# Kernel optimization log

Measured on AMD Instinct MI355X. Metric: run time of the kernel, lower is better.

## Reference

```python
import jax, jax.numpy as jnp
from jax import lax
import numpy as np

B, H, W = 8, 160, 256
C, K = 700, 250
N_BINS = 750
N_HIST, N_JIT = 30, 60
N_FRAMES = N_HIST + N_JIT
MAGIC = 400.0 / (750.0 - 500.0 + 500.0)


def setup_inputs() -> dict:
    key = jax.random.key(0)
    ks = jax.random.split(key, 10)
    n_pix = H * W
    return {
        "batched_image": jax.random.normal(ks[0], (B, H, W), jnp.float32),
        "batched_spikes": jax.random.uniform(ks[1], (B, C, N_BINS), jnp.float32),
        "eye_movements": jax.random.randint(ks[2], (B, N_JIT, 2), 0, 15),
        "time_mask": jax.random.uniform(ks[3], (B, N_BINS - K), jnp.float32),
        "forward_sel": jax.random.randint(ks[4], (B, N_BINS, 2), 0, N_FRAMES),
        "forward_weights": jax.random.uniform(ks[5], (B, N_BINS, 2), jnp.float32),
        # scale filters so the generator signal stays O(1) under exp() nonlinearity
        "stacked_flat_spat_filters": jax.random.normal(ks[6], (C, n_pix), jnp.float32) / np.sqrt(n_pix).astype(np.float32),
        "stacked_timecourse_filters": jax.random.normal(ks[7], (C, K), jnp.float32) / np.sqrt(K).astype(np.float32),
        "precomputed_feedback_gensig": 0.1 * jax.random.normal(ks[8], (B, C, N_BINS - K + 1), jnp.float32),
        "precomputed_history_frames": jax.random.normal(ks[9], (B, N_HIST, C), jnp.float32),
    }


def _jitter(image, eye_movements):
    # image: (B,H,W); eye_movements: (B,F,2) int shifts. Gather with zero fill.
    dy, dx = eye_movements[..., 0], eye_movements[..., 1]
    rows = jnp.arange(H)[None, None, :] + dy[:, :, None]      # (B,F,H)
    cols = jnp.arange(W)[None, None, :] + dx[:, :, None]      # (B,F,W)
    vr = (rows >= 0) & (rows < H)
    vc = (cols >= 0) & (cols < W)
    rc = jnp.clip(rows, 0, H - 1)
    cc = jnp.clip(cols, 0, W - 1)
    bidx = jnp.arange(image.shape[0])[:, None, None, None]
    jit = image[bidx, rc[:, :, :, None], cc[:, :, None, :]]   # (B,F,H,W)
    mask = (vr[:, :, :, None] & vc[:, :, None, :]).astype(image.dtype)
    return jit * mask


def reference(batched_image, batched_spikes, eye_movements, time_mask,
              forward_sel, forward_weights, stacked_flat_spat_filters,
              stacked_timecourse_filters, precomputed_feedback_gensig,
              precomputed_history_frames):
    b = batched_image.shape[0]
    # eye-movement jitter (gather)
    jit = _jitter(batched_image, eye_movements)                       # (B,Fj,H,W)
    jit_flat = jit.reshape(b, -1, H * W)                              # (B,Fj,P)
    spat_j = jnp.einsum('cp,bfp->bfc', stacked_flat_spat_filters, jit_flat)
    spat = jnp.concatenate([precomputed_history_frames, spat_j], axis=1)  # (B,Ftot,C)
    # interval-overlap time upsample: each bin mixes <=2 frames
    t = forward_sel.shape[1]
    gath = jnp.take_along_axis(spat, forward_sel.reshape(b, t * 2, 1), axis=1)
    gath = gath.reshape(b, t, 2, -1)                                  # (B,T,2,C)
    upsampled = jnp.einsum('btjc,btj->bct', gath, forward_weights)    # (B,C,T)
    # grouped (depthwise) conv1d, valid, no flip (cross-correlation like torch)
    time_filt = lax.conv_general_dilated(
        upsampled, stacked_timecourse_filters[:, None, :],
        window_strides=(1,), padding='VALID',
        dimension_numbers=('NCH', 'OIH', 'NCH'), feature_group_count=C)  # (B,C,T-K+1)
    gen_sig = time_filt + precomputed_feedback_gensig
    g = gen_sig[:, :, :-1]
    s = batched_spikes[:, :, K:]
    loss = jnp.exp(g) - s * g                                          # Poisson NLL (unnormed)
    loss = loss * time_mask[:, None, :] * MAGIC
    return jnp.sum(loss, axis=(1, 2))
```

## Files before the change

### kernel.cpp

```cpp
#include <hip/hip_runtime.h>
#include <hip/hip_bf16.h>
#include <math.h>

#define BB    8
#define HH    160
#define WW    256
#define CC    700
#define KK    250
#define NBINS 750
#define NHIST 30
#define NJIT  60
#define NFRM  90
#define PP    (HH*WW)
#define TOUT  500
#define MAGIC (400.0f/750.0f)

#define MPAD   512
#define NPAD   768
#define KPTOT  640
#define KSPLIT 32
#define KPZ    20
#define BSCALE     64.0f
#define INV_BSCALE (1.0f/64.0f)
#define PA_BLKS (32*20)
#define PB_BLKS (48*20)

typedef __attribute__((ext_vector_type(8))) short short8;
typedef __attribute__((ext_vector_type(4))) float f32x4;

__device__ __forceinline__ unsigned char f2fp8(float x) {
    x = fminf(fmaxf(x, -440.f), 440.f);
    unsigned u = __builtin_bit_cast(unsigned, x);
    unsigned s = (u >> 24) & 0x80u;
    int e = (u >> 23) & 0xFF;
    if (e < 121) return (unsigned char)s;
    unsigned u2 = u + 0x7FFFFu + ((u >> 20) & 1u);
    int e2 = (u2 >> 23) & 0xFF;
    unsigned m = (u2 >> 20) & 7u;
    if (e2 > 135 || (e2 == 135 && m == 7u)) return (unsigned char)(s | 0x7E);
    return (unsigned char)(s | ((unsigned)(e2 - 120) << 3) | m);
}

__device__ __forceinline__ unsigned pk4_fp8(float a, float b, float c, float d) {
#if __has_builtin(__builtin_amdgcn_cvt_pk_fp8_f32)
    int v = __builtin_amdgcn_cvt_pk_fp8_f32(a, b, 0, false);
    v = __builtin_amdgcn_cvt_pk_fp8_f32(c, d, v, true);
    return (unsigned)v;
#else
    return (unsigned)f2fp8(a) | ((unsigned)f2fp8(b) << 8)
         | ((unsigned)f2fp8(c) << 16) | ((unsigned)f2fp8(d) << 24);
#endif
}

__device__ __forceinline__ void gload16(const void* g, void* l) {
    __builtin_amdgcn_global_load_lds(
        (const __attribute__((address_space(1))) unsigned int*)g,
        (__attribute__((address_space(3))) unsigned int*)l, 16, 0, 0);
}

__device__ __forceinline__ int SWZ(int X) { return X ^ (((X >> 8) & 7) << 4); }

__device__ __forceinline__ int FRX(int r, int pl) {
    return ((pl >> 6) << 10) | ((((pl >> 3) & 3) * 16 + r) << 4)
         | (((pl >> 5) & 1) << 3) | (pl & 7);
}

__global__ __launch_bounds__(256) void pack_ab(
    const float* __restrict__ img, const int* __restrict__ eye,
    const float* __restrict__ filt,
    unsigned char* __restrict__ Ap, unsigned char* __restrict__ Bp)
{
    __shared__ unsigned char lds[8192];
    const int t = threadIdx.x, w = t >> 6, l = t & 63;
    const int bid = blockIdx.x;

    if (bid < PA_BLKS) {
        const int mt = bid / 20, ch4 = bid % 20;
        int rbv[4], rdy[4], rdx[4]; bool rok[4];
        #pragma unroll
        for (int sub = 0; sub < 4; ++sub) {
            int r = sub*4 + w, m = mt*16 + r;
            rok[sub] = (m < 480);
            int b = 0, dy = 0, dx = 0;
            if (rok[sub]) {
                b = m / 60; int f = m % 60;
                dy = eye[(b*NJIT + f)*2 + 0];
                dx = eye[(b*NJIT + f)*2 + 1];
            }
            rbv[sub] = b; rdy[sub] = dy; rdx[sub] = dx;
        }
        for (int q = 0; q < 4; ++q) {
            const int ch = ch4*4 + q;
            const int kbase = ch * 512;
            #pragma unroll
            for (int sub = 0; sub < 4; ++sub) {
                const int r = sub*4 + w;
                const float* imgb = img + (size_t)rbv[sub]*PP;
                const int dx = rdx[sub];
                #pragma unroll
                for (int h = 0; h < 2; ++h) {
                    const int ir = (kbase >> 8) + h + rdy[sub];
                    const bool ok = rok[sub] && (ir < HH);
                    float4 v = make_float4(0.f,0.f,0.f,0.f);
                    if (ok) v = *(const float4*)(imgb + ir*WW + 4*l);
                    unsigned pk = pk4_fp8(v.x, v.y, v.z, v.w);
                    const int plb = h*256;
                    if (!ok || l >= 60)
                        *(unsigned*)(lds + SWZ(FRX(r, plb + 4*l))) = 0u;
                    if (ok) {
                        #pragma unroll
                        for (int j = 0; j < 4; ++j) {
                            int pc = 4*l + j - dx;
                            if (pc >= 0)
                                lds[SWZ(FRX(r, plb + pc))] =
                                    (unsigned char)(pk >> (8*j));
                        }
                    }
                }
            }
            __syncthreads();
            unsigned char* outp = Ap + ((size_t)mt*KPTOT + ch*8)*1024;
            #pragma unroll
            for (int i = 0; i < 2; ++i) {
                int X = i*4096 + t*16;
                short8 v = *(const short8*)(lds + SWZ(X));
                *(short8*)(outp + X) = v;
            }
            __syncthreads();
        }
    } else {
        const int bb = bid - PA_BLKS;
        const int nt = bb / 20, ch4 = bb % 20;
        for (int q = 0; q < 4; ++q) {
            const int ch = ch4*4 + q;
            const int kbase = ch * 512;
            #pragma unroll
            for (int sub = 0; sub < 4; ++sub) {
                int r = sub*4 + w, n = nt*16 + r;
                float4 va = make_float4(0.f,0.f,0.f,0.f), vb = va;
                if (n < CC) {
                    const float* rowp = filt + (size_t)n*PP + kbase;
                    va = *(const float4*)(rowp + l*4);
                    vb = *(const float4*)(rowp + l*4 + 256);
                }
                unsigned da = pk4_fp8(va.x*BSCALE, va.y*BSCALE, va.z*BSCALE, va.w*BSCALE);
                unsigned db = pk4_fp8(vb.x*BSCALE, vb.y*BSCALE, vb.z*BSCALE, vb.w*BSCALE);
                int Xa = FRX(r, 4*l);
                *(unsigned*)(lds + SWZ(Xa)) = da;
                *(unsigned*)(lds + SWZ(Xa + (4 << 10))) = db;
            }
            __syncthreads();
            unsigned char* outp = Bp + ((size_t)nt*KPTOT + ch*8)*1024;
            #pragma unroll
            for (int i = 0; i < 2; ++i) {
                int X = i*4096 + t*16;
                short8 v = *(const short8*)(lds + SWZ(X));
                *(short8*)(outp + X) = v;
            }
            __syncthreads();
        }
    }
}

__global__ __launch_bounds__(256) void gemm_f8(
    const unsigned char* __restrict__ Ap, const unsigned char* __restrict__ Bp,
    __hip_bfloat16* __restrict__ part)
{
    __shared__ unsigned char As[8192];
    __shared__ unsigned char Bs[8192];

    const int t = threadIdx.x, l = t & 63, w = t >> 6;
    const int bid = blockIdx.x;
    const int g   = bid >> 3;
    const int z   = (bid & 7) + 8*(g / 24);
    const int tt  = g % 24;
    const int mtile = tt / 6, ntile = tt % 6;
    const int wr = w >> 1, wc = w & 1;

    f32x4 acc[4][4] = {};

    for (int step = 0; step < KPZ; ++step) {
        const size_t kp = (size_t)z*KPZ + step;
        const int tb0 = w*2, tb1 = w*2 + 1;
        gload16(Ap + ((size_t)(mtile*8 + tb0)*KPTOT + kp)*1024 + l*16, As + tb0*1024);
        gload16(Ap + ((size_t)(mtile*8 + tb1)*KPTOT + kp)*1024 + l*16, As + tb1*1024);
        gload16(Bp + ((size_t)(ntile*8 + tb0)*KPTOT + kp)*1024 + l*16, Bs + tb0*1024);
        gload16(Bp + ((size_t)(ntile*8 + tb1)*KPTOT + kp)*1024 + l*16, Bs + tb1*1024);
        __syncthreads();

        ulonglong2 a[4], b[4];
        #pragma unroll
        for (int i = 0; i < 4; ++i)
            a[i] = *(const ulonglong2*)(As + (wr*4 + i)*1024 + l*16);
        #pragma unroll
        for (int j = 0; j < 4; ++j)
            b[j] = *(const ulonglong2*)(Bs + (wc*4 + j)*1024 + l*16);
        #pragma unroll
        for (int i = 0; i < 4; ++i)
            #pragma unroll
            for (int j = 0; j < 4; ++j) {
                acc[i][j] = __builtin_amdgcn_mfma_f32_16x16x32_fp8_fp8(
                    (long long)a[i].x, (long long)b[j].x, acc[i][j], 0, 0, 0);
                acc[i][j] = __builtin_amdgcn_mfma_f32_16x16x32_fp8_fp8(
                    (long long)a[i].y, (long long)b[j].y, acc[i][j], 0, 0, 0);
            }
        __syncthreads();
    }

    const int rbase = (l >> 4)*4, cl = l & 15;
    #pragma unroll
    for (int i = 0; i < 4; ++i)
        #pragma unroll
        for (int j = 0; j < 4; ++j) {
            int m = mtile*128 + wr*64 + i*16 + rbase;
            int n = ntile*128 + wc*64 + j*16 + cl;
            __hip_bfloat16* p = part + ((size_t)z*MPAD + m)*NPAD + n;
            #pragma unroll
            for (int r = 0; r < 4; ++r)
                p[(size_t)r*NPAD] = __float2bfloat16(acc[i][j][r]);
        }
}

__global__ __launch_bounds__(256) void build_spat(
    const float* __restrict__ hist, const __hip_bfloat16* __restrict__ part,
    float* __restrict__ spatT)
{
    int idx = blockIdx.x*256 + threadIdx.x;
    if (idx >= BB*NFRM*CC) return;
    int c   = idx % CC;
    int rem = idx / CC;
    int fr  = rem % NFRM;
    int b   = rem / NFRM;
    float v;
    if (fr < NHIST) {
        v = hist[(b*NHIST + fr)*CC + c];
    } else {
        int m = b*NJIT + (fr - NHIST);
        v = 0.f;
        #pragma unroll
        for (int kp = 0; kp < KSPLIT; ++kp)
            v += __bfloat162float(part[((size_t)kp*MPAD + m)*NPAD + c]);
        v *= INV_BSCALE;
    }
    spatT[((size_t)b*CC + c)*NFRM + fr] = v;
}

__global__ __launch_bounds__(64) void conv_loss(
    const float* __restrict__ spatT, const int* __restrict__ sel,
    const float* __restrict__ wts,  const float* __restrict__ tc,
    const float* __restrict__ fb,   const float* __restrict__ spk,
    const float* __restrict__ tmask, float* __restrict__ lpart)
{
    __shared__ float tcs[256];
    __shared__ float spc[96];
    __shared__ float ups[864];

    const int lane = threadIdx.x;
    const int c = blockIdx.x;
    const int b = blockIdx.y;

    for (int k = lane; k < 256; k += 64)
        tcs[k] = (k < KK) ? tc[c*KK + k] : 0.f;
    {
        const float* spT = spatT + (size_t)(b*CC + c)*NFRM;
        for (int i = lane; i < NFRM; i += 64) spc[i] = spT[i];
    }
    __syncthreads();

    for (int tt = lane; tt < 768; tt += 64) {
        float v = 0.f;
        if (tt < NBINS) {
            int base = (b*NBINS + tt);
            int2   s2 = *(const int2*)  (sel + base*2);
            float2 w2 = *(const float2*)(wts + base*2);
            v = w2.x * spc[s2.x] + w2.y * spc[s2.y];
        }
        ups[tt + (tt >> 3)] = v;
    }
    __syncthreads();

    const int t0 = lane * 8;
    float u[16];
    #pragma unroll
    for (int j = 0; j < 16; ++j) { int q = t0 + j; u[j] = ups[q + (q >> 3)]; }

    float acc[8] = {};
    #pragma unroll 4
    for (int kc = 0; kc < 248; kc += 8) {
        #pragma unroll
        for (int kk = 0; kk < 8; ++kk) {
            float w2 = tcs[kc + kk];
            #pragma unroll
            for (int j = 0; j < 8; ++j) acc[j] += w2 * u[kk + j];
        }
        #pragma unroll
        for (int j = 0; j < 8; ++j) u[j] = u[j + 8];
        #pragma unroll
        for (int j = 0; j < 8; ++j) {
            int q = t0 + kc + 16 + j;
            u[j + 8] = ups[q + (q >> 3)];
        }
    }
    #pragma unroll
    for (int kk = 0; kk < 8; ++kk) {
        float w2 = tcs[248 + kk];
        #pragma unroll
        for (int j = 0; j < 8; ++j) acc[j] += w2 * u[kk + j];
    }

    const size_t bc = (size_t)b*CC + c;
    const float* fbp = fb  + bc*(TOUT+1);
    const float* sp  = spk + bc*NBINS + KK;
    const float* tm  = tmask + (size_t)b*TOUT;
    float lsum = 0.f;
    #pragma unroll
    for (int j = 0; j < 8; ++j) {
        int tt = t0 + j;
        if (tt < TOUT) {
            float g  = acc[j] + fbp[tt];
            float sv = sp[tt];
            lsum += (__expf(g) - sv*g) * tm[tt];
        }
    }
    #pragma unroll
    for (int off = 32; off > 0; off >>= 1)
        lsum += __shfl_down(lsum, off);
    if (lane == 0) lpart[bc] = lsum * MAGIC;
}

__global__ __launch_bounds__(256) void reduce_out(
    const float* __restrict__ lpart, float* __restrict__ out)
{
    __shared__ float red[256];
    int b = blockIdx.x, t = threadIdx.x;
    float s = 0.f;
    for (int i = t; i < CC; i += 256) s += lpart[(size_t)b*CC + i];
    red[t] = s; __syncthreads();
    for (int o = 128; o > 0; o >>= 1) {
        if (t < o) red[t] += red[t+o];
        __syncthreads();
    }
    if (t == 0) out[b] = red[0];
}

extern "C" void kernel_launch(void* const* d_in, const int* in_sizes, int n_in,
                              void* d_out, int out_size, void* d_ws, size_t ws_size,
                              hipStream_t stream) {
    const float* image = (const float*)d_in[0];
    const float* spk   = (const float*)d_in[1];
    const int*   eye   = (const int*)d_in[2];
    const float* tmask = (const float*)d_in[3];
    const int*   sel   = (const int*)d_in[4];
    const float* wts   = (const float*)d_in[5];
    const float* filt  = (const float*)d_in[6];
    const float* tc    = (const float*)d_in[7];
    const float* fb    = (const float*)d_in[8];
    const float* hist  = (const float*)d_in[9];
    float* out = (float*)d_out;

    unsigned char* Ap = (unsigned char*)d_ws;
    unsigned char* Bp = Ap + (size_t)32*KPTOT*1024;
    __hip_bfloat16* part = (__hip_bfloat16*)(Bp + (size_t)48*KPTOT*1024);
    float* spatT = (float*)(part + (size_t)KSPLIT*MPAD*NPAD);
    float* lpart = spatT + (size_t)BB*NFRM*CC;

    pack_ab  <<<dim3(PA_BLKS + PB_BLKS), 256, 0, stream>>>(image, eye, filt, Ap, Bp);
    gemm_f8  <<<dim3(8*96), 256, 0, stream>>>(Ap, Bp, part);
    build_spat<<<dim3((BB*NFRM*CC + 255)/256), 256, 0, stream>>>(hist, part, spatT);
    conv_loss<<<dim3(CC, BB), 64, 0, stream>>>(spatT, sel, wts, tc, fb, spk, tmask, lpart);
    reduce_out<<<dim3(BB), 256, 0, stream>>>(lpart, out);
}
```

Baseline: 103.9 us.

## Fuse final reduction into conv_loss and rebalance pack block granularity

The final per-batch reduction kernel is removed. conv_loss now uses an atomic completion counter so the last block for each batch sums the partials and writes the output. A memset is added to clear the counter before each run. The pack kernel now launches twice as many blocks, each handling 2 chunks instead of 4, and schedules the heavier filter-packing blocks first to improve load balance and occupancy. This adds a memset launch and atomic traffic in exchange for dropping one kernel launch.

```diff
diff --git a/kernel.cpp b/kernel.cpp
--- a/kernel.cpp
+++ b/kernel.cpp
@@ -22,8 +22,8 @@
 #define KPZ    20
 #define BSCALE     64.0f
 #define INV_BSCALE (1.0f/64.0f)
-#define PA_BLKS (32*20)
-#define PB_BLKS (48*20)
+#define PB_BLKS (48*40)
+#define PA_BLKS (32*40)
 
 typedef __attribute__((ext_vector_type(8))) short short8;
 typedef __attribute__((ext_vector_type(4))) float f32x4;
@@ -74,8 +74,39 @@
     const int t = threadIdx.x, w = t >> 6, l = t & 63;
     const int bid = blockIdx.x;
 
-    if (bid < PA_BLKS) {
-        const int mt = bid / 20, ch4 = bid % 20;
+    if (bid < PB_BLKS) {
+        const int nt = bid / 40, ch2 = bid % 40;
+        for (int q = 0; q < 2; ++q) {
+            const int ch = ch2*2 + q;
+            const int kbase = ch * 512;
+            #pragma unroll
+            for (int sub = 0; sub < 4; ++sub) {
+                int r = sub*4 + w, n = nt*16 + r;
+                float4 va = make_float4(0.f,0.f,0.f,0.f), vb = va;
+                if (n < CC) {
+                    const float* rowp = filt + (size_t)n*PP + kbase;
+                    va = *(const float4*)(rowp + l*4);
+                    vb = *(const float4*)(rowp + l*4 + 256);
+                }
+                unsigned da = pk4_fp8(va.x*BSCALE, va.y*BSCALE, va.z*BSCALE, va.w*BSCALE);
+                unsigned db = pk4_fp8(vb.x*BSCALE, vb.y*BSCALE, vb.z*BSCALE, vb.w*BSCALE);
+                int Xa = FRX(r, 4*l);
+                *(unsigned*)(lds + SWZ(Xa)) = da;
+                *(unsigned*)(lds + SWZ(Xa + (4 << 10))) = db;
+            }
+            __syncthreads();
+            unsigned char* outp = Bp + ((size_t)nt*KPTOT + ch*8)*1024;
+            #pragma unroll
+            for (int i = 0; i < 2; ++i) {
+                int X = i*4096 + t*16;
+                short8 v = *(const short8*)(lds + SWZ(X));
+                *(short8*)(outp + X) = v;
+            }
+            __syncthreads();
+        }
+    } else {
+        const int aid = bid - PB_BLKS;
+        const int mt = aid / 40, ch2 = aid % 40;
         int rbv[4], rdy[4], rdx[4]; bool rok[4];
         #pragma unroll
         for (int sub = 0; sub < 4; ++sub) {
@@ -89,9 +120,8 @@
             }
             rbv[sub] = b; rdy[sub] = dy; rdx[sub] = dx;
         }
-        for (int q = 0; q < 4; ++q) {
-            const int ch = ch4*4 + q;
-            const int kbase = ch * 512;
+        for (int q = 0; q < 2; ++q) {
+            const int ch = ch2*2 + q;
             #pragma unroll
             for (int sub = 0; sub < 4; ++sub) {
                 const int r = sub*4 + w;
@@ -99,7 +129,7 @@
                 const int dx = rdx[sub];
                 #pragma unroll
                 for (int h = 0; h < 2; ++h) {
-                    const int ir = (kbase >> 8) + h + rdy[sub];
+                    const int ir = ch*2 + h + rdy[sub];
                     const bool ok = rok[sub] && (ir < HH);
                     float4 v = make_float4(0.f,0.f,0.f,0.f);
                     if (ok) v = *(const float4*)(imgb + ir*WW + 4*l);
@@ -128,37 +158,6 @@
             }
             __syncthreads();
         }
-    } else {
-        const int bb = bid - PA_BLKS;
-        const int nt = bb / 20, ch4 = bb % 20;
-        for (int q = 0; q < 4; ++q) {
-            const int ch = ch4*4 + q;
-            const int kbase = ch * 512;
-            #pragma unroll
-            for (int sub = 0; sub < 4; ++sub) {
-                int r = sub*4 + w, n = nt*16 + r;
-                float4 va = make_float4(0.f,0.f,0.f,0.f), vb = va;
-                if (n < CC) {
-                    const float* rowp = filt + (size_t)n*PP + kbase;
-                    va = *(const float4*)(rowp + l*4);
-                    vb = *(const float4*)(rowp + l*4 + 256);
-                }
-                unsigned da = pk4_fp8(va.x*BSCALE, va.y*BSCALE, va.z*BSCALE, va.w*BSCALE);
-                unsigned db = pk4_fp8(vb.x*BSCALE, vb.y*BSCALE, vb.z*BSCALE, vb.w*BSCALE);
-                int Xa = FRX(r, 4*l);
-                *(unsigned*)(lds + SWZ(Xa)) = da;
-                *(unsigned*)(lds + SWZ(Xa + (4 << 10))) = db;
-            }
-            __syncthreads();
-            unsigned char* outp = Bp + ((size_t)nt*KPTOT + ch*8)*1024;
-            #pragma unroll
-            for (int i = 0; i < 2; ++i) {
-                int X = i*4096 + t*16;
-                short8 v = *(const short8*)(lds + SWZ(X));
-                *(short8*)(outp + X) = v;
-            }
-            __syncthreads();
-        }
     }
 }
 
@@ -249,7 +248,8 @@
     const float* __restrict__ spatT, const int* __restrict__ sel,
     const float* __restrict__ wts,  const float* __restrict__ tc,
     const float* __restrict__ fb,   const float* __restrict__ spk,
-    const float* __restrict__ tmask, float* __restrict__ lpart)
+    const float* __restrict__ tmask, float* __restrict__ lpart,
+    int* __restrict__ done, float* __restrict__ out)
 {
     __shared__ float tcs[256];
     __shared__ float spc[96];
@@ -325,22 +325,25 @@
     #pragma unroll
     for (int off = 32; off > 0; off >>= 1)
         lsum += __shfl_down(lsum, off);
-    if (lane == 0) lpart[bc] = lsum * MAGIC;
-}
-
-__global__ __launch_bounds__(256) void reduce_out(
-    const float* __restrict__ lpart, float* __restrict__ out)
-{
-    __shared__ float red[256];
-    int b = blockIdx.x, t = threadIdx.x;
-    float s = 0.f;
-    for (int i = t; i < CC; i += 256) s += lpart[(size_t)b*CC + i];
-    red[t] = s; __syncthreads();
-    for (int o = 128; o > 0; o >>= 1) {
-        if (t < o) red[t] += red[t+o];
-        __syncthreads();
-    }
-    if (t == 0) out[b] = red[0];
+
+    __shared__ int sDoLast;
+    if (lane == 0) {
+        lpart[bc] = lsum * MAGIC;
+        __threadfence();
+        int prev = atomicAdd(&done[b], 1);
+        sDoLast = (prev == CC - 1);
+    }
+    __syncthreads();
+    if (sDoLast) {
+        __threadfence();
+        const float* lp = lpart + (size_t)b*CC;
+        float s = 0.f;
+        for (int i = lane; i < CC; i += 64) s += lp[i];
+        #pragma unroll
+        for (int off = 32; off > 0; off >>= 1)
+            s += __shfl_down(s, off);
+        if (lane == 0) out[b] = s;
+    }
 }
 
 extern "C" void kernel_launch(void* const* d_in, const int* in_sizes, int n_in,
@@ -363,10 +366,12 @@
     __hip_bfloat16* part = (__hip_bfloat16*)(Bp + (size_t)48*KPTOT*1024);
     float* spatT = (float*)(part + (size_t)KSPLIT*MPAD*NPAD);
     float* lpart = spatT + (size_t)BB*NFRM*CC;
-
-    pack_ab  <<<dim3(PA_BLKS + PB_BLKS), 256, 0, stream>>>(image, eye, filt, Ap, Bp);
+    int*   done  = (int*)(lpart + (size_t)BB*CC);
+
+    hipMemsetAsync(done, 0, BB*sizeof(int), stream);
+    pack_ab  <<<dim3(PB_BLKS + PA_BLKS), 256, 0, stream>>>(image, eye, filt, Ap, Bp);
     gemm_f8  <<<dim3(8*96), 256, 0, stream>>>(Ap, Bp, part);
     build_spat<<<dim3((BB*NFRM*CC + 255)/256), 256, 0, stream>>>(hist, part, spatT);
-    conv_loss<<<dim3(CC, BB), 64, 0, stream>>>(spatT, sel, wts, tc, fb, spk, tmask, lpart);
-    reduce_out<<<dim3(BB), 256, 0, stream>>>(lpart, out);
-}
+    conv_loss<<<dim3(CC, BB), 64, 0, stream>>>(spatT, sel, wts, tc, fb, spk, tmask,
+                                               lpart, done, out);
+}
```

New measurement: 215.4 us. +107.3%, slower.
